# Optimization experiments

Measured on AMD Instinct MI355X. Metric: run time of the kernel, lower is better.

Reference implementation:

```python
import jax, jax.numpy as jnp
import numpy as np

B, T, V, E, H = 1024, 256, 90, 8, 256


def setup_inputs() -> dict:
    key = jax.random.key(0)
    ks = jax.random.split(key, 40)
    rn = lambda k, shape: jax.random.normal(k, shape, dtype=jnp.float32) * 0.05
    inp = {}
    inp["input_seq"] = jax.random.randint(ks[0], (B, T), 0, V, dtype=jnp.int32)
    inp["emb"] = rn(ks[1], (V, E)).at[0].set(0.0)  # padding_idx=0
    i = 2
    for name, din in [("g1", E), ("g2", H), ("l1", E), ("l2", H)]:
        inp[name + "_Wih"] = rn(ks[i], (4 * H, din)); i += 1
        inp[name + "_Whh"] = rn(ks[i], (4 * H, H)); i += 1
        inp[name + "_bih"] = rn(ks[i], (4 * H,)); i += 1
        inp[name + "_bhh"] = rn(ks[i], (4 * H,)); i += 1
    for name in ["p1", "p2"]:
        inp[name + "_W1"] = rn(ks[i], (2 * H, E + 4 * H)); i += 1
        inp[name + "_b1"] = rn(ks[i], (2 * H,)); i += 1
        inp[name + "_W2"] = rn(ks[i], (H, 2 * H)); i += 1
        inp[name + "_b2"] = rn(ks[i], (H,)); i += 1
        inp[name + "_W3"] = rn(ks[i], (2, H)); i += 1
        inp[name + "_b3"] = rn(ks[i], (2,)); i += 1
    inp["gfc_W"] = rn(ks[i], (V, H)); i += 1
    inp["gfc_b"] = rn(ks[i], (V,)); i += 1
    inp["lfc_W"] = rn(ks[i], (V, H)); i += 1
    inp["lfc_b"] = rn(ks[i], (V,))
    return inp


def _cell(x, h, c, Wih, Whh, bih, bhh):
    # PyTorch LSTMCell: gate order i, f, g, o
    g = x @ Wih.T + h @ Whh.T + (bih + bhh)
    i, f, gg, o = jnp.split(g, 4, axis=-1)
    c = jax.nn.sigmoid(f) * c + jax.nn.sigmoid(i) * jnp.tanh(gg)
    return jax.nn.sigmoid(o) * jnp.tanh(c), c


def _mlp(x, W1, b1, W2, b2, W3, b3):
    h = jax.nn.relu(x @ W1.T + b1)
    h = jax.nn.relu(h @ W2.T + b2)
    return h @ W3.T + b3


def _forward(input_seq, emb,
             g1_Wih, g1_Whh, g1_bih, g1_bhh, g2_Wih, g2_Whh, g2_bih, g2_bhh,
             l1_Wih, l1_Whh, l1_bih, l1_bhh, l2_Wih, l2_Whh, l2_bih, l2_bhh,
             p1_W1, p1_b1, p1_W2, p1_b2, p1_W3, p1_b3,
             p2_W1, p2_b1, p2_W2, p2_b2, p2_W3, p2_b3,
             gfc_W, gfc_b, lfc_W, lfc_b):
    Bn = input_seq.shape[0]
    embeds = emb[input_seq]  # [B, T, E]
    z = jnp.zeros((Bn, H), dtype=emb.dtype)

    def step(carry, e):
        gh1, gc1, gh2, gc2, lh1, lc1, lh2, lc2 = carry
        gh1, gc1 = _cell(e, gh1, gc1, g1_Wih, g1_Whh, g1_bih, g1_bhh)
        lh1, lc1 = _cell(e, lh1, lc1, l1_Wih, l1_Whh, l1_bih, l1_bhh)
        p = jax.nn.softmax(_mlp(jnp.concatenate([e, gh1, gc1, lh1, lc1], 1),
                                p1_W1, p1_b1, p1_W2, p1_b2, p1_W3, p1_b3), axis=1)
        # bmm([B,1,2],[B,2,H]) == p0*local + p1*global
        gh1 = p[:, 0:1] * lh1 + p[:, 1:2] * gh1
        gc1 = p[:, 0:1] * lc1 + p[:, 1:2] * gc1
        gh2, gc2 = _cell(gh1, gh2, gc2, g2_Wih, g2_Whh, g2_bih, g2_bhh)
        lh2, lc2 = _cell(lh1, lh2, lc2, l2_Wih, l2_Whh, l2_bih, l2_bhh)
        p = jax.nn.softmax(_mlp(jnp.concatenate([e, gh2, gc2, lh2, lc2], 1),
                                p2_W1, p2_b1, p2_W2, p2_b2, p2_W3, p2_b3), axis=1)
        gh2 = p[:, 0:1] * lh2 + p[:, 1:2] * gh2
        gc2 = p[:, 0:1] * lc2 + p[:, 1:2] * gc2
        return (gh1, gc1, gh2, gc2, lh1, lc1, lh2, lc2), gh2

    _, hs = jax.lax.scan(step, (z, z, z, z, z, z, z, z), jnp.swapaxes(embeds, 0, 1))
    hs = jnp.swapaxes(hs, 0, 1)  # [B, T, H]
    out = 0.5 * (hs @ gfc_W.T + gfc_b) + 0.5 * (hs @ lfc_W.T + lfc_b)
    return jnp.swapaxes(out, 1, 2)  # [B, V, T]


def reference(input_seq, emb,
              g1_Wih, g1_Whh, g1_bih, g1_bhh, g2_Wih, g2_Whh, g2_bih, g2_bhh,
              l1_Wih, l1_Whh, l1_bih, l1_bhh, l2_Wih, l2_Whh, l2_bih, l2_bhh,
              p1_W1, p1_b1, p1_W2, p1_b2, p1_W3, p1_b3,
              p2_W1, p2_b1, p2_W2, p2_b2, p2_W3, p2_b3,
              gfc_W, gfc_b, lfc_W, lfc_b):
    return _forward(input_seq, emb,
                    g1_Wih, g1_Whh, g1_bih, g1_bhh, g2_Wih, g2_Whh, g2_bih, g2_bhh,
                    l1_Wih, l1_Whh, l1_bih, l1_bhh, l2_Wih, l2_Whh, l2_bih, l2_bhh,
                    p1_W1, p1_b1, p1_W2, p1_b2, p1_W3, p1_b3,
                    p2_W1, p2_b1, p2_W2, p2_b2, p2_W3, p2_b3,
                    gfc_W, gfc_b, lfc_W, lfc_b)
```

## Files before the change

### kernel.cpp

```cpp
#include <hip/hip_runtime.h>

#define B_ 1024
#define T_ 256
#define V_ 90
#define H_ 256
#define NTHR 512
#define NBLK 256
#define S_ ((size_t)B_*H_)
#define HS_ (S_/2)

typedef unsigned short u16;
typedef __attribute__((ext_vector_type(8))) _Float16 f16x8;
typedef __attribute__((ext_vector_type(4))) _Float16 f16x4;
typedef __attribute__((ext_vector_type(4))) float f32x4;

constexpr size_t OFF_GH1C  = 0;
constexpr size_t OFF_GH1P  = OFF_GH1C + HS_;
constexpr size_t OFF_LH1   = OFF_GH1P + HS_;
constexpr size_t OFF_GH2C  = OFF_LH1 + 2*HS_;
constexpr size_t OFF_GH2P  = OFF_GH2C + HS_;
constexpr size_t OFF_LH2   = OFF_GH2P + HS_;
constexpr size_t OFF_GC1PH = OFF_LH2 + 2*HS_;
constexpr size_t OFF_LC1H  = OFF_GC1PH + HS_;
constexpr size_t OFF_GC2PH = OFF_LC1H + 2*HS_;
constexpr size_t OFF_LC2H  = OFF_GC2PH + HS_;
constexpr size_t OFF_GC1C  = OFF_LC2H + 2*HS_;
constexpr size_t OFF_GC1P  = OFF_GC1C + S_;
constexpr size_t OFF_LC1   = OFF_GC1P + S_;
constexpr size_t OFF_GC2C  = OFF_LC1 + 2*S_;
constexpr size_t OFF_GC2P  = OFF_GC2C + S_;
constexpr size_t OFF_LC2   = OFF_GC2P + S_;
constexpr size_t OFF_M1H   = OFF_LC2 + 2*S_;
constexpr size_t OFF_M2H   = OFF_M1H + (size_t)B_*512/2;
constexpr size_t OFF_OSTG  = OFF_M2H + (size_t)B_*512/2;
constexpr size_t OFF_EX    = OFF_OSTG + (size_t)B_*16*90;
constexpr size_t OFF_WG1PK = OFF_EX + 2*B_*8;
constexpr size_t OFF_WE1   = OFF_WG1PK + 256*2048/2;
constexpr size_t OFF_BG1   = OFF_WE1 + 8*2048;
constexpr size_t OFF_WL2PK = OFF_BG1 + 2048;
constexpr size_t OFF_BL2   = OFF_WL2PK + 512*1024/2;
constexpr size_t OFF_WG2PK = OFF_BL2 + 1024;
constexpr size_t OFF_BG2   = OFF_WG2PK + 512*1024/2;
constexpr size_t OFF_WP1PK = OFF_BG2 + 1024;
constexpr size_t OFF_WEP1  = OFF_WP1PK + 1024*512/2;
constexpr size_t OFF_WP2PK = OFF_WEP1 + 8*512;
constexpr size_t OFF_WEP2  = OFF_WP2PK + 1024*512/2;
constexpr size_t OFF_WB1   = OFF_WEP2 + 8*512;
constexpr size_t OFF_WB2   = OFF_WB1 + 512*256/2;
constexpr size_t OFF_WOUT  = OFF_WB2 + 512*256/2;
constexpr size_t OFF_BOUT  = OFF_WOUT + 256*96;
constexpr size_t OFF_BAR   = OFF_BOUT + 128;
constexpr size_t WS_FLOATS = OFF_BAR + 8192;

struct InP {
  const int*   seq;
  const float* emb;
  const float *g1_Wih,*g1_Whh,*g1_bih,*g1_bhh;
  const float *g2_Wih,*g2_Whh,*g2_bih,*g2_bhh;
  const float *l1_Wih,*l1_Whh,*l1_bih,*l1_bhh;
  const float *l2_Wih,*l2_Whh,*l2_bih,*l2_bhh;
  const float *p1_W1,*p1_b1,*p1_W2,*p1_b2,*p1_W3,*p1_b3;
  const float *p2_W1,*p2_b1,*p2_W2,*p2_b2,*p2_W3,*p2_b3;
  const float *gfc_W,*gfc_b,*lfc_W,*lfc_b;
};

__device__ __forceinline__ float sig_(float x)  { return 1.f/(1.f+__expf(-x)); }
__device__ __forceinline__ float tanh_(float x) { return 1.f - 2.f/(__expf(2.f*x)+1.f); }
__device__ __forceinline__ u16 f2h(float v) {
  _Float16 h = (_Float16)v; return __builtin_bit_cast(unsigned short, h);
}

__device__ __forceinline__ unsigned ld_flag(const unsigned* p) {
  unsigned v;
  asm volatile("global_load_dword %0, %1, off sc1\n\ts_waitcnt vmcnt(0)"
               : "=v"(v) : "v"(p) : "memory");
  return v;
}
__device__ __forceinline__ void st_flag(unsigned* p, unsigned v) {
  asm volatile("global_store_dword %0, %1, off sc1\n\ts_waitcnt vmcnt(0)"
               :: "v"(p), "v"(v) : "memory");
}

__device__ __forceinline__ void gbar_x(unsigned* arr, int slot, unsigned ep)
{
  __syncthreads();
  if (threadIdx.x == 0) st_flag(&arr[slot*16], ep);
  if (threadIdx.x < 32) {
    int cap = 0;
    for (;;) {
      unsigned v = ld_flag(&arr[threadIdx.x*16]);
      if (v >= ep) break;
      __builtin_amdgcn_s_sleep(1);
      if (++cap > 200000) break;
    }
  }
  __syncthreads();
  asm volatile("buffer_inv sc0" ::: "memory");
}

__device__ __forceinline__ void gl_lds16(const void* g, void* l) {
  __builtin_amdgcn_global_load_lds(
      (const __attribute__((address_space(1))) unsigned int*)g,
      (__attribute__((address_space(3))) unsigned int*)l, 16, 0, 2);
}
__device__ __forceinline__ void dma64(const u16* src, u16* dstbase) {
  const int wv = threadIdx.x >> 6, lane = threadIdx.x & 63;
  const char* g = (const char*)src + lane*16;
  char* l = (char*)dstbase;
#pragma unroll
  for (int j = 0; j < 8; ++j) {
    const int ofs = (wv*8 + j) * 1024;
    gl_lds16(g + ofs, l + ofs);
  }
}

template<int NCH, int NSEG, bool HASE, int TPW, class FE>
__device__ __forceinline__ void mm_lds(
    const u16* bufp,
    const u16* s0, const u16* s1_, const u16* s2_, const u16* s3_,
    const float* WeP, int ldwe, const float* ex,
    int rows0, int ct0, FE fe)
{
  const int tid = threadIdx.x, lane = tid & 63, wr = tid >> 6;
  const int row = rows0 + wr*16 + (lane & 15);
  const int kq  = (lane >> 4) << 3;

  f32x4 acc[TPW];
#pragma unroll
  for (int t = 0; t < TPW; ++t) acc[t] = (f32x4){0,0,0,0};

  constexpr int DEP = (NCH < 8) ? NCH : 8;
  f16x8 areg[DEP];
  auto ldA = [&](int c) -> f16x8 {
    const int k0 = c * 32;
    const u16* S;
    if (NSEG == 1) S = s0;
    else if (NSEG == 2) S = (k0 < 256) ? s0 : s1_;
    else S = (k0 < 256) ? s0 : (k0 < 512) ? s1_ : (k0 < 768) ? s2_ : s3_;
    return *(const f16x8*)&S[(size_t)row*H_ + (k0 & 255) + kq];
  };

#pragma unroll
  for (int c = 0; c < DEP; ++c) areg[c] = ldA(c);
#pragma unroll
  for (int c = 0; c < NCH; ++c) {
    f16x8 a = areg[c % DEP];
#pragma unroll
    for (int t = 0; t < TPW; ++t) {
      f16x8 b = *(const f16x8*)(bufp + (size_t)(c*TPW + t)*512 + lane*8);
      acc[t] = __builtin_amdgcn_mfma_f32_16x16x32_f16(a, b, acc[t], 0, 0, 0);
    }
    if (c + DEP < NCH) areg[c % DEP] = ldA(c + DEP);
  }

  if (HASE) {
#pragma unroll
    for (int t = 0; t < TPW; ++t) {
      const int colL = ct0 + t*16 + (lane & 15);
      float w[8];
#pragma unroll
      for (int j = 0; j < 8; ++j) w[j] = WeP[j*ldwe + colL];
#pragma unroll
      for (int m = 0; m < 4; ++m) {
        const int rr = rows0 + wr*16 + ((lane >> 4) << 2) + m;
        float s = 0.f;
#pragma unroll
        for (int j = 0; j < 8; ++j) s = __builtin_fmaf(ex[rr*8 + j], w[j], s);
        acc[t][m] += s;
      }
    }
  }
  fe(wr, lane, acc);
}

template<int TPW>
struct GateEpiM {
  const float* cin; u16* ho; float* co; u16* coh; const float* bias_pk;
  int rows0; int ct0;
  __device__ void operator()(int wr, int lane, f32x4 (&acc)[TPW]) const {
    const int rbase = rows0 + wr*16 + ((lane >> 4) << 2);
#pragma unroll
    for (int gi = 0; gi < TPW/4; ++gi) {
      const int cb = ct0 + gi*64;
      const int h = (((cb & 1023) >> 6) << 4) + (lane & 15);
      float b[4];
#pragma unroll
      for (int t = 0; t < 4; ++t) b[t] = bias_pk[cb + t*16 + (lane & 15)];
#pragma unroll
      for (int m = 0; m < 4; ++m) {
        const size_t ix = (size_t)(rbase + m)*H_ + h;
        float gI = sig_(acc[gi*4+0][m] + b[0]);
        float gF = sig_(acc[gi*4+1][m] + b[1]);
        float gG = tanh_(acc[gi*4+2][m] + b[2]);
        float gO = sig_(acc[gi*4+3][m] + b[3]);
        float cn = gF*cin[ix] + gI*gG;
        ho[ix] = f2h(gO*tanh_(cn));
        co[ix] = cn;
        coh[ix] = f2h(cn);
      }
    }
  }
};

struct MlpEpiH {
  u16* dst; const float* b1; int rows0; int ct0;
  __device__ void operator()(int wr, int lane, f32x4 (&acc)[2]) const {
    const int rbase = rows0 + wr*16 + ((lane >> 4) << 2);
#pragma unroll
    for (int t = 0; t < 2; ++t) {
      const int c = ct0 + t*16 + (lane & 15);
      const float bb = b1[c];
#pragma unroll
      for (int m = 0; m < 4; ++m)
        dst[(size_t)(rbase + m)*512 + c] = f2h(fmaxf(acc[t][m] + bb, 0.f));
    }
  }
};

__device__ __forceinline__ void stage_F2(
    int rowbase,
    const u16* M, const u16* WBpk, const float* b2,
    const float* W3, const float* b3,
    const u16* lh, const float* lc,
    const u16* ghp, const float* gcp,
    u16* ghc, float* gcc)
{
  const int w = threadIdx.x >> 6, lane = threadIdx.x & 63;
  const int r0 = rowbase + w*2;
  const u16* a0 = M + (size_t)r0*512;
  const u16* a1 = a0 + 512;
  float m0[4] = {0.f,0.f,0.f,0.f}, m1[4] = {0.f,0.f,0.f,0.f};
  for (int k0 = 0; k0 < 512; k0 += 4) {
    f16x4 x0 = *(const f16x4*)&a0[k0];
    f16x4 x1 = *(const f16x4*)&a1[k0];
#pragma unroll
    for (int j = 0; j < 4; ++j) {
      f16x4 wv = *(const f16x4*)&WBpk[(size_t)(k0+j)*256 + lane*4];
      float w0 = (float)wv[0], w1 = (float)wv[1], w2 = (float)wv[2], w3v = (float)wv[3];
      float xv0 = (float)x0[j], xv1 = (float)x1[j];
      m0[0] = __builtin_fmaf(xv0, w0, m0[0]);
      m0[1] = __builtin_fmaf(xv0, w1, m0[1]);
      m0[2] = __builtin_fmaf(xv0, w2, m0[2]);
      m0[3] = __builtin_fmaf(xv0, w3v, m0[3]);
      m1[0] = __builtin_fmaf(xv1, w0, m1[0]);
      m1[1] = __builtin_fmaf(xv1, w1, m1[1]);
      m1[2] = __builtin_fmaf(xv1, w2, m1[2]);
      m1[3] = __builtin_fmaf(xv1, w3v, m1[3]);
    }
  }
  float4 b = *(const float4*)&b2[lane*4];
  float bb2[4] = {b.x,b.y,b.z,b.w};
#pragma unroll
  for (int j = 0; j < 4; ++j) {
    m0[j] = fmaxf(m0[j]+bb2[j], 0.f);
    m1[j] = fmaxf(m1[j]+bb2[j], 0.f);
  }
  float4 w30 = *(const float4*)&W3[lane*4];
  float4 w31 = *(const float4*)&W3[256 + lane*4];
  float w0v[4] = {w30.x,w30.y,w30.z,w30.w};
  float w1v[4] = {w31.x,w31.y,w31.z,w31.w};
  float d00=0.f, d01=0.f, d10=0.f, d11=0.f;
#pragma unroll
  for (int j = 0; j < 4; ++j) {
    d00 = __builtin_fmaf(m0[j], w0v[j], d00);
    d01 = __builtin_fmaf(m0[j], w1v[j], d01);
    d10 = __builtin_fmaf(m1[j], w0v[j], d10);
    d11 = __builtin_fmaf(m1[j], w1v[j], d11);
  }
#pragma unroll
  for (int off = 32; off; off >>= 1) {
    d00 += __shfl_xor(d00, off, 64); d01 += __shfl_xor(d01, off, 64);
    d10 += __shfl_xor(d10, off, 64); d11 += __shfl_xor(d11, off, 64);
  }
  d00 += b3[0]; d01 += b3[1]; d10 += b3[0]; d11 += b3[1];
  float mxa = fmaxf(d00, d01), mxb = fmaxf(d10, d11);
  float e00 = __expf(d00-mxa), e01 = __expf(d01-mxa);
  float e10 = __expf(d10-mxb), e11 = __expf(d11-mxb);
  float ia = 1.f/(e00+e01), ib = 1.f/(e10+e11);
  float p0a = e00*ia, p1a = e01*ia;
  float p0b = e10*ib, p1b = e11*ib;
#pragma unroll
  for (int rr = 0; rr < 2; ++rr) {
    const float p0 = rr ? p0b : p0a, p1 = rr ? p1b : p1a;
    const size_t ix = (size_t)(r0+rr)*H_ + lane*4;
    f16x4 lv = *(const f16x4*)&lh[ix];
    f16x4 gv = *(const f16x4*)&ghp[ix];
    f16x4 oh;
#pragma unroll
    for (int j = 0; j < 4; ++j)
      oh[j] = (_Float16)(p0*(float)lv[j] + p1*(float)gv[j]);
    *(f16x4*)&ghc[ix] = oh;
    float4 lcv = *(const float4*)&lc[ix];
    float4 gcv = *(const float4*)&gcp[ix];
    float4 oc;
    oc.x = p0*lcv.x + p1*gcv.x; oc.y = p0*lcv.y + p1*gcv.y;
    oc.z = p0*lcv.z + p1*gcv.z; oc.w = p0*lcv.w + p1*gcv.w;
    *(float4*)&gcc[ix] = oc;
  }
}

__device__ __forceinline__ void stage_OUTS(
    const u16* gh2c, const float* WOUT, const float* BOUT,
    float* ostg, int rbase, int tt)
{
  const int w = threadIdx.x >> 6, lane = threadIdx.x & 63;
  const bool two = lane < (V_ - 64);
#pragma unroll
  for (int rr = 0; rr < 2; ++rr) {
    const int r = rbase + w*2 + rr;
    const u16* arow = gh2c + (size_t)r * H_;
    float acc0 = 0.f, acc1 = 0.f;
    for (int k0 = 0; k0 < 256; k0 += 8) {
      f16x8 a8 = *(const f16x8*)&arow[k0];
#pragma unroll
      for (int j = 0; j < 8; ++j) {
        const float av = (float)a8[j];
        const float* wr_ = &WOUT[(size_t)(k0+j)*96];
        acc0 = __builtin_fmaf(av, wr_[lane], acc0);
        if (two) acc1 = __builtin_fmaf(av, wr_[64+lane], acc1);
      }
    }
    float* dst = &ostg[((size_t)r*16 + (tt & 15))*90];
    dst[lane] = acc0 + BOUT[lane];
    if (two) dst[64+lane] = acc1 + BOUT[64+lane];
  }
}

__device__ __forceinline__ void flush_out(
    const float* ostg, float* out, int rbase, int tb0)
{
  for (int i = threadIdx.x; i < 16*90; i += NTHR) {
    const int rr = i / 90, v = i - rr*90;
    const int r = rbase + rr;
    const float* src = &ostg[((size_t)r*16)*90 + v];
    float tmp[16];
#pragma unroll
    for (int tb = 0; tb < 16; ++tb) tmp[tb] = src[tb*90];
    float* dst = &out[((size_t)r*V_ + v)*T_ + tb0];
#pragma unroll
    for (int q = 0; q < 4; ++q)
      ((float4*)dst)[q] = make_float4(tmp[q*4], tmp[q*4+1], tmp[q*4+2], tmp[q*4+3]);
  }
}

__global__ void k_setup(InP in, float* __restrict__ ws)
{
  const size_t nthr = (size_t)gridDim.x * blockDim.x;
  const size_t t0 = (size_t)blockIdx.x * blockDim.x + threadIdx.x;

  for (size_t i = t0; i < OFF_M1H; i += nthr) ws[i] = 0.f;
  for (size_t i = t0; i < 8192; i += nthr) ((unsigned*)(ws + OFF_BAR))[i] = 0u;

  for (size_t i = t0; i < (size_t)B_*8; i += nthr) {
    int r = (int)(i >> 3), j = (int)(i & 7);
    ws[OFF_EX + i] = in.emb[(size_t)in.seq[(size_t)r*T_]*8 + j];
  }

  {
    u16* dst = (u16*)(ws + OFF_WG1PK);
    for (size_t i = t0; i < (size_t)16*8*8*512; i += nthr) {
      int e = (int)(i & 7), lane = (int)((i >> 3) & 63);
      int tile = (int)((i >> 9) & 7), ck = (int)((i >> 12) & 7), blk = (int)(i >> 15);
      int col = blk*128 + tile*16 + (lane & 15);
      int k = ck*32 + ((lane >> 4) << 3) + e;
      int cell = col >> 10, q = col & 1023;
      int h = ((q >> 6) << 4) + (q & 15), g = (q >> 4) & 3, R = g*256 + h;
      dst[i] = f2h((cell ? in.l1_Whh : in.g1_Whh)[(size_t)R*256 + k]);
    }
  }
  for (size_t i = t0; i < (size_t)8*2048; i += nthr) {
    int j = (int)(i >> 11), p = (int)(i & 2047);
    int cell = p >> 10, q = p & 1023;
    int h = ((q >> 6) << 4) + (q & 15), g = (q >> 4) & 3, R = g*256 + h;
    ws[OFF_WE1 + (size_t)j*2048 + p] = (cell ? in.l1_Wih : in.g1_Wih)[(size_t)R*8 + j];
  }
  for (size_t i = t0; i < 2048; i += nthr) {
    int p = (int)i, cell = p >> 10, q = p & 1023;
    int h = ((q >> 6) << 4) + (q & 15), g = (q >> 4) & 3, R = g*256 + h;
    ws[OFF_BG1 + i] = cell ? (in.l1_bih[R] + in.l1_bhh[R]) : (in.g1_bih[R] + in.g1_bhh[R]);
  }

  for (int which = 0; which < 2; ++which) {
    u16* dst = (u16*)(ws + (which ? OFF_WG2PK : OFF_WL2PK));
    const float* Wih = which ? in.g2_Wih : in.l2_Wih;
    const float* Whh = which ? in.g2_Whh : in.l2_Whh;
    for (size_t i = t0; i < (size_t)16*16*4*512; i += nthr) {
      int e = (int)(i & 7), lane = (int)((i >> 3) & 63);
      int tile = (int)((i >> 9) & 3), ck = (int)((i >> 11) & 15), blk = (int)(i >> 15);
      int col = blk*64 + tile*16 + (lane & 15);
      int k = ck*32 + ((lane >> 4) << 3) + e;
      int h = ((col >> 6) << 4) + (col & 15), g = (col >> 4) & 3, R = g*256 + h;
      float w = (k < 256) ? Wih[(size_t)R*256 + k] : Whh[(size_t)R*256 + (k-256)];
      dst[i] = f2h(w);
    }
  }
  for (size_t i = t0; i < 2*1024; i += nthr) {
    int which = (int)(i >> 10), p = (int)(i & 1023);
    int h = ((p >> 6) << 4) + (p & 15), g = (p >> 4) & 3, R = g*256 + h;
    float v = which ? (in.g2_bih[R] + in.g2_bhh[R]) : (in.l2_bih[R] + in.l2_bhh[R]);
    ws[(which ? OFF_BG2 : OFF_BL2) + p] = v;
  }

  for (int which = 0; which < 2; ++which) {
    u16* dst = (u16*)(ws + (which ? OFF_WP2PK : OFF_WP1PK));
    const float* W = which ? in.p2_W1 : in.p1_W1;
    for (size_t i = t0; i < (size_t)16*32*2*512; i += nthr) {
      int e = (int)(i & 7), lane = (int)((i >> 3) & 63);
      int tile = (int)((i >> 9) & 1), ck = (int)((i >> 10) & 31), blk = (int)(i >> 15);
      int col = blk*32 + tile*16 + (lane & 15);
      int k = ck*32 + ((lane >> 4) << 3) + e;
      dst[i] = f2h(W[(size_t)col*1032 + 8 + k]);
    }
  }
  for (size_t i = t0; i < (size_t)2*8*512; i += nthr) {
    int which = (int)(i / (8*512));
    int idx = (int)(i - (size_t)which*8*512);
    int j = idx >> 9, p = idx & 511;
    const float* W = which ? in.p2_W1 : in.p1_W1;
    ws[(which ? OFF_WEP2 : OFF_WEP1) + (size_t)j*512 + p] = W[(size_t)p*1032 + j];
  }

  for (size_t i = t0; i < (size_t)2*512*256; i += nthr) {
    int which = (int)(i / (512*256));
    int idx = (int)(i - (size_t)which*512*256);
    int k = idx >> 8, n = idx & 255;
    const float* W = which ? in.p2_W2 : in.p1_W2;
    ((u16*)(ws + (which ? OFF_WB2 : OFF_WB1)))[idx] = f2h(W[(size_t)n*512 + k]);
  }
  for (size_t i = t0; i < (size_t)256*96; i += nthr) {
    int k = (int)(i / 96), c = (int)(i - (size_t)k*96);
    float v = 0.f;
    if (c < V_) v = 0.5f*(in.gfc_W[(size_t)c*256 + k] + in.lfc_W[(size_t)c*256 + k]);
    ws[OFF_WOUT + i] = v;
  }
  for (size_t i = t0; i < 96; i += nthr)
    ws[OFF_BOUT + i] = (i < V_) ? 0.5f*(in.gfc_b[i] + in.lfc_b[i]) : 0.f;
}

__global__ __launch_bounds__(NTHR) void k_main(InP in, float* ws, float* __restrict__ out)
{
  __shared__ __attribute__((aligned(16))) u16 sB0[32768];
  extern __shared__ u16 dynB[];
  __shared__ unsigned s_slot;

  u16*  GH1C = (u16*)(ws + OFF_GH1C);
  u16*  GH1P = (u16*)(ws + OFF_GH1P);
  u16*  LH1  = (u16*)(ws + OFF_LH1);
  u16*  GH2C = (u16*)(ws + OFF_GH2C);
  u16*  GH2P = (u16*)(ws + OFF_GH2P);
  u16*  LH2  = (u16*)(ws + OFF_LH2);
  u16*  GC1PH= (u16*)(ws + OFF_GC1PH);
  u16*  LC1H = (u16*)(ws + OFF_LC1H);
  u16*  GC2PH= (u16*)(ws + OFF_GC2PH);
  u16*  LC2H = (u16*)(ws + OFF_LC2H);
  float* GC1C = ws + OFF_GC1C;  float* GC1P = ws + OFF_GC1P;
  float* LC1  = ws + OFF_LC1;
  float* GC2C = ws + OFF_GC2C;  float* GC2P = ws + OFF_GC2P;
  float* LC2  = ws + OFF_LC2;
  u16*   M1H  = (u16*)(ws + OFF_M1H);
  u16*   M2H  = (u16*)(ws + OFF_M2H);
  float* OSTG = ws + OFF_OSTG;
  float* EXB  = ws + OFF_EX;
  const u16* WG1PK = (const u16*)(ws + OFF_WG1PK);
  const u16* WL2PK = (const u16*)(ws + OFF_WL2PK);
  const u16* WG2PK = (const u16*)(ws + OFF_WG2PK);
  const u16* WP1PK = (const u16*)(ws + OFF_WP1PK);
  const u16* WP2PK = (const u16*)(ws + OFF_WP2PK);
  const u16* WB1PK = (const u16*)(ws + OFF_WB1);
  const u16* WB2PK = (const u16*)(ws + OFF_WB2);
  const float* WE1  = ws + OFF_WE1;  const float* BG1P = ws + OFF_BG1;
  const float* BL2P = ws + OFF_BL2;  const float* BG2P = ws + OFF_BG2;
  const float* WEP1 = ws + OFF_WEP1; const float* WEP2 = ws + OFF_WEP2;
  const float* WOUT = ws + OFF_WOUT; const float* BOUT = ws + OFF_BOUT;

  unsigned xcc;
  asm volatile("s_getreg_b32 %0, hwreg(HW_REG_XCC_ID)" : "=s"(xcc));
  xcc &= 7u;
  unsigned* barx = ((unsigned*)(ws + OFF_BAR)) + xcc*1024;
  unsigned* arr  = barx;
  unsigned* reg  = barx + 544;
  if (threadIdx.x == 0)
    s_slot = __hip_atomic_fetch_add(reg, 1u, __ATOMIC_RELAXED, __HIP_MEMORY_SCOPE_AGENT);
  __syncthreads();
  const int slot  = (int)(s_slot & 31u);
  const int rows0 = (int)xcc * 128;
  const int s2 = slot & 15;
  unsigned ep = 0;
  int wb = 0;

  if (slot < 16) dma64(WG1PK + (size_t)slot*32768, sB0);
  else           dma64(WG2PK + (size_t)s2*32768, sB0);
  asm volatile("s_waitcnt vmcnt(0)" ::: "memory");
  __syncthreads();

  for (int n = 0; n <= T_; ++n) {
    const int sel = n & 1;
    const float* ex  = EXB + sel*(B_*8);
    const float* exm = EXB + (sel^1)*(B_*8);
    u16* lh1o = LH1 + sel*(B_*H_);   u16* lh1n = LH1 + (sel^1)*(B_*H_);
    float* lc1o = LC1 + sel*S_;      float* lc1n = LC1 + (sel^1)*S_;
    u16* lc1nh = LC1H + (sel^1)*(B_*H_);
    u16* lh2o = LH2 + sel*(B_*H_);   u16* lh2n = LH2 + (sel^1)*(B_*H_);
    float* lc2o = LC2 + sel*S_;      float* lc2n = LC2 + (sel^1)*S_;
    u16* lc2oh = LC2H + sel*(B_*H_); u16* lc2nh = LC2H + (sel^1)*(B_*H_);

    u16* bC; u16* bF;

    bC = wb ? dynB : sB0; bF = wb ? sB0 : dynB;
    if (slot < 16) dma64(WP1PK + (size_t)s2*32768, bF);
    else           dma64(WP2PK + (size_t)s2*32768, bF);
    if (slot < 16) {
      if (n < T_) {
        const int ct0 = slot*128;
        const int cell = slot >> 3;
        GateEpiM<8> epi{ cell ? lc1o : GC1C,
                         cell ? lh1n : GH1P,
                         cell ? lc1n : GC1P,
                         cell ? lc1nh : GC1PH,
                         BG1P, rows0, ct0 };
        mm_lds<8,1,true,8>(bC, cell ? lh1o : GH1C, nullptr, nullptr, nullptr,
                           WE1, 2048, ex, rows0, ct0, epi);
      }
    } else if (n >= 1) {
      const int ct0 = s2*64;
      GateEpiM<4> epi{ GC2C, GH2P, GC2P, GC2PH, BG2P, rows0, ct0 };
      mm_lds<16,2,false,4>(bC, GH1C, GH2C, nullptr, nullptr,
                           nullptr, 0, nullptr, rows0, ct0, epi);
    }
    gbar_x(arr, slot, ++ep);
    wb ^= 1;

    bC = wb ? dynB : sB0; bF = wb ? sB0 : dynB;
    if (slot < 16) dma64(WL2PK + (size_t)slot*32768, bF);
    else           dma64(WG2PK + (size_t)s2*32768, bF);
    if (slot < 16) {
      if (n < T_) {
        const int ct0 = s2*32;
        MlpEpiH epi{ M1H, in.p1_b1, rows0, ct0 };
        mm_lds<32,4,true,2>(bC, GH1P, GC1PH, lh1n, lc1nh,
                            WEP1, 512, ex, rows0, ct0, epi);
      }
    } else if (n >= 1) {
      const int ct0 = s2*32;
      MlpEpiH epi{ M2H, in.p2_b1, rows0, ct0 };
      mm_lds<32,4,true,2>(bC, GH2P, GC2PH, lh2o, lc2oh,
                          WEP2, 512, exm, rows0, ct0, epi);
    }
    gbar_x(arr, slot, ++ep);
    wb ^= 1;

    bC = wb ? dynB : sB0; bF = wb ? sB0 : dynB;
    if (slot < 16) {
      dma64(WG1PK + (size_t)slot*32768, bF);
      if (n < T_) {
        const int ct0 = slot*64;
        GateEpiM<4> epi{ lc2o, lh2n, lc2n, lc2nh, BL2P, rows0, ct0 };
        mm_lds<16,2,false,4>(bC, lh1n, lh2o, nullptr, nullptr,
                             nullptr, 0, nullptr, rows0, ct0, epi);
      }
    } else if (slot < 24) {
      if (n < T_) {
        const int rb = rows0 + (slot-16)*16;
        stage_F2(rb, M1H, WB1PK, in.p1_b2, in.p1_W3, in.p1_b3,
                 lh1n, lc1n, GH1P, GC1P, GH1C, GC1C);
        if (n + 1 < T_ && threadIdx.x < 128) {
          const int r = rb + (threadIdx.x >> 3), j = threadIdx.x & 7;
          EXB[(sel^1)*(B_*8) + r*8 + j] =
              in.emb[(size_t)in.seq[(size_t)r*T_ + n + 1]*8 + j];
        }
      }
    } else {
      if (n >= 1) {
        const int rb = rows0 + (slot-24)*16;
        stage_F2(rb, M2H, WB2PK, in.p2_b2, in.p2_W3, in.p2_b3,
                 lh2o, lc2o, GH2P, GC2P, GH2C, GC2C);
        __syncthreads();
        stage_OUTS(GH2C, WOUT, BOUT, OSTG, rb, n-1);
        if (((n-1) & 15) == 15) {
          __syncthreads();
          flush_out(OSTG, out, rb, n-16);
        }
      }
    }
    gbar_x(arr, slot, ++ep);
    if (slot < 16) wb ^= 1;
  }
}

extern "C" void kernel_launch(void* const* d_in, const int* in_sizes, int n_in,
                              void* d_out, int out_size, void* d_ws, size_t ws_size,
                              hipStream_t stream)
{
  if (ws_size < WS_FLOATS * sizeof(float)) return;

  InP in;
  in.seq    = (const int*)  d_in[0];
  in.emb    = (const float*)d_in[1];
  in.g1_Wih = (const float*)d_in[2];  in.g1_Whh = (const float*)d_in[3];
  in.g1_bih = (const float*)d_in[4];  in.g1_bhh = (const float*)d_in[5];
  in.g2_Wih = (const float*)d_in[6];  in.g2_Whh = (const float*)d_in[7];
  in.g2_bih = (const float*)d_in[8];  in.g2_bhh = (const float*)d_in[9];
  in.l1_Wih = (const float*)d_in[10]; in.l1_Whh = (const float*)d_in[11];
  in.l1_bih = (const float*)d_in[12]; in.l1_bhh = (const float*)d_in[13];
  in.l2_Wih = (const float*)d_in[14]; in.l2_Whh = (const float*)d_in[15];
  in.l2_bih = (const float*)d_in[16]; in.l2_bhh = (const float*)d_in[17];
  in.p1_W1  = (const float*)d_in[18]; in.p1_b1  = (const float*)d_in[19];
  in.p1_W2  = (const float*)d_in[20]; in.p1_b2  = (const float*)d_in[21];
  in.p1_W3  = (const float*)d_in[22]; in.p1_b3  = (const float*)d_in[23];
  in.p2_W1  = (const float*)d_in[24]; in.p2_b1  = (const float*)d_in[25];
  in.p2_W2  = (const float*)d_in[26]; in.p2_b2  = (const float*)d_in[27];
  in.p2_W3  = (const float*)d_in[28]; in.p2_b3  = (const float*)d_in[29];
  in.gfc_W  = (const float*)d_in[30]; in.gfc_b  = (const float*)d_in[31];
  in.lfc_W  = (const float*)d_in[32]; in.lfc_b  = (const float*)d_in[33];

  float* ws  = (float*)d_ws;
  float* out = (float*)d_out;

  k_setup<<<512, 256, 0, stream>>>(in, ws);
  k_main <<<NBLK, NTHR, 65536, stream>>>(in, ws, out);
}
```

Baseline: 56.92 ms.

## Replicate packed weights per XCC and drop cache-policy bits on LDS loads

Adds a kernel that copies the five packed weight blobs into eight per-XCC replicas, so each XCC's blocks stream weights into LDS from their own copy rather than all contending for one shared copy. It also changes the global_load_lds cache-policy argument from 2 to 0, which alters caching behaviour on each weight reload. The replication path is used only when the workspace is large enough. It costs a roughly 40 MB extra copy per launch and more workspace, and the gain depends on whether the shared-copy reads were actually contended.

New measurement: 55.89 ms. Within noise of the previous version (-1.8%).

```diff
diff --git a/kernel.cpp b/kernel.cpp
--- a/kernel.cpp
+++ b/kernel.cpp
@@ -50,7 +50,10 @@
 constexpr size_t OFF_WOUT  = OFF_WB2 + 512*256/2;
 constexpr size_t OFF_BOUT  = OFF_WOUT + 256*96;
 constexpr size_t OFF_BAR   = OFF_BOUT + 128;
-constexpr size_t WS_FLOATS = OFF_BAR + 8192;
+constexpr size_t OFF_WREP  = OFF_BAR + 8192;
+constexpr size_t WS_FLOATS = OFF_WREP;
+constexpr size_t REP_U32   = (size_t)5*262144;
+constexpr size_t WS_FULL   = OFF_WREP + 8*REP_U32;
 
 struct InP {
   const int*   seq;
@@ -101,7 +104,7 @@
 __device__ __forceinline__ void gl_lds16(const void* g, void* l) {
   __builtin_amdgcn_global_load_lds(
       (const __attribute__((address_space(1))) unsigned int*)g,
-      (__attribute__((address_space(3))) unsigned int*)l, 16, 0, 2);
+      (__attribute__((address_space(3))) unsigned int*)l, 16, 0, 0);
 }
 __device__ __forceinline__ void dma64(const u16* src, u16* dstbase) {
   const int wv = threadIdx.x >> 6, lane = threadIdx.x & 63;
@@ -437,7 +440,22 @@
     ws[OFF_BOUT + i] = (i < V_) ? 0.5f*(in.gfc_b[i] + in.lfc_b[i]) : 0.f;
 }
 
-__global__ __launch_bounds__(NTHR) void k_main(InP in, float* ws, float* __restrict__ out)
+__global__ void k_rep(float* __restrict__ ws)
+{
+  const size_t nthr = (size_t)gridDim.x * blockDim.x;
+  const size_t t0 = (size_t)blockIdx.x * blockDim.x + threadIdx.x;
+  unsigned* dst0 = (unsigned*)(ws + OFF_WREP);
+  for (size_t i = t0; i < (size_t)8*REP_U32; i += nthr) {
+    const size_t rep = i / REP_U32, q = i - rep*REP_U32;
+    const size_t blob = q / 262144, w = q - blob*262144;
+    const size_t src_off = (blob == 0) ? OFF_WG1PK : (blob == 1) ? OFF_WL2PK :
+                           (blob == 2) ? OFF_WG2PK : (blob == 3) ? OFF_WP1PK : OFF_WP2PK;
+    dst0[i] = ((const unsigned*)(ws + src_off))[w];
+  }
+}
+
+__global__ __launch_bounds__(NTHR) void k_main(InP in, float* ws, float* __restrict__ out,
+                                               int use_rep)
 {
   __shared__ __attribute__((aligned(16))) u16 sB0[32768];
   extern __shared__ u16 dynB[];
@@ -461,11 +479,6 @@
   u16*   M2H  = (u16*)(ws + OFF_M2H);
   float* OSTG = ws + OFF_OSTG;
   float* EXB  = ws + OFF_EX;
-  const u16* WG1PK = (const u16*)(ws + OFF_WG1PK);
-  const u16* WL2PK = (const u16*)(ws + OFF_WL2PK);
-  const u16* WG2PK = (const u16*)(ws + OFF_WG2PK);
-  const u16* WP1PK = (const u16*)(ws + OFF_WP1PK);
-  const u16* WP2PK = (const u16*)(ws + OFF_WP2PK);
   const u16* WB1PK = (const u16*)(ws + OFF_WB1);
   const u16* WB2PK = (const u16*)(ws + OFF_WB2);
   const float* WE1  = ws + OFF_WE1;  const float* BG1P = ws + OFF_BG1;
@@ -476,6 +489,14 @@
   unsigned xcc;
   asm volatile("s_getreg_b32 %0, hwreg(HW_REG_XCC_ID)" : "=s"(xcc));
   xcc &= 7u;
+
+  const u16* WR = (const u16*)(ws + OFF_WREP) + (size_t)xcc * (5u*524288u);
+  const u16* WG1X = use_rep ? WR             : (const u16*)(ws + OFF_WG1PK);
+  const u16* WL2X = use_rep ? WR + 524288u   : (const u16*)(ws + OFF_WL2PK);
+  const u16* WG2X = use_rep ? WR + 1048576u  : (const u16*)(ws + OFF_WG2PK);
+  const u16* WP1X = use_rep ? WR + 1572864u  : (const u16*)(ws + OFF_WP1PK);
+  const u16* WP2X = use_rep ? WR + 2097152u  : (const u16*)(ws + OFF_WP2PK);
+
   unsigned* barx = ((unsigned*)(ws + OFF_BAR)) + xcc*1024;
   unsigned* arr  = barx;
   unsigned* reg  = barx + 544;
@@ -488,8 +509,8 @@
   unsigned ep = 0;
   int wb = 0;
 
-  if (slot < 16) dma64(WG1PK + (size_t)slot*32768, sB0);
-  else           dma64(WG2PK + (size_t)s2*32768, sB0);
+  if (slot < 16) dma64(WG1X + (size_t)slot*32768, sB0);
+  else           dma64(WG2X + (size_t)s2*32768, sB0);
   asm volatile("s_waitcnt vmcnt(0)" ::: "memory");
   __syncthreads();
 
@@ -507,8 +528,8 @@
     u16* bC; u16* bF;
 
     bC = wb ? dynB : sB0; bF = wb ? sB0 : dynB;
-    if (slot < 16) dma64(WP1PK + (size_t)s2*32768, bF);
-    else           dma64(WP2PK + (size_t)s2*32768, bF);
+    if (slot < 16) dma64(WP1X + (size_t)s2*32768, bF);
+    else           dma64(WP2X + (size_t)s2*32768, bF);
     if (slot < 16) {
       if (n < T_) {
         const int ct0 = slot*128;
@@ -531,8 +552,8 @@
     wb ^= 1;
 
     bC = wb ? dynB : sB0; bF = wb ? sB0 : dynB;
-    if (slot < 16) dma64(WL2PK + (size_t)slot*32768, bF);
-    else           dma64(WG2PK + (size_t)s2*32768, bF);
+    if (slot < 16) dma64(WL2X + (size_t)slot*32768, bF);
+    else           dma64(WG2X + (size_t)s2*32768, bF);
     if (slot < 16) {
       if (n < T_) {
         const int ct0 = s2*32;
@@ -551,7 +572,7 @@
 
     bC = wb ? dynB : sB0; bF = wb ? sB0 : dynB;
     if (slot < 16) {
-      dma64(WG1PK + (size_t)slot*32768, bF);
+      dma64(WG1X + (size_t)slot*32768, bF);
       if (n < T_) {
         const int ct0 = slot*64;
         GateEpiM<4> epi{ lc2o, lh2n, lc2n, lc2nh, BL2P, rows0, ct0 };
@@ -592,6 +613,7 @@
                               hipStream_t stream)
 {
   if (ws_size < WS_FLOATS * sizeof(float)) return;
+  const int use_rep = (ws_size >= WS_FULL * sizeof(float)) ? 1 : 0;
 
   InP in;
   in.seq    = (const int*)  d_in[0];
@@ -617,5 +639,6 @@
   float* out = (float*)d_out;
 
   k_setup<<<512, 256, 0, stream>>>(in, ws);
-  k_main <<<NBLK, NTHR, 65536, stream>>>(in, ws, out);
-}
+  if (use_rep) k_rep<<<512, 256, 0, stream>>>(ws);
+  k_main <<<NBLK, NTHR, 65536, stream>>>(in, ws, out, use_rep);
+}
```
